# Performance work log

Measured on AMD Instinct MI355X. Metric: run time of the kernel, lower is better.

## Reference

```python
import jax, jax.numpy as jnp
import numpy as np

IN_FEATURES = 4096
OUT_FEATURES = 11008
QMIN, QMAX = -128, 127


def setup_inputs() -> dict:
    key = jax.random.key(0)
    k_in, k_w, k_s, k_z, k_b = jax.random.split(key, 5)
    inp = jax.random.normal(k_in, (4, 2048, IN_FEATURES), dtype=jnp.float32)
    # int8 quantized weight in [qmin, qmax]
    weight_quantized = jax.random.randint(
        k_w, (OUT_FEATURES, IN_FEATURES), QMIN, QMAX + 1, dtype=jnp.int32
    ).astype(jnp.int8)
    # per-output-row scale / zero point (shape [out, 1] as in the module)
    weight_scale = jax.random.uniform(k_s, (OUT_FEATURES, 1), dtype=jnp.float32,
                                      minval=0.005, maxval=0.02)
    weight_zero_point = jax.random.uniform(k_z, (OUT_FEATURES, 1), dtype=jnp.float32,
                                           minval=-4.0, maxval=4.0)
    bias = jax.random.normal(k_b, (OUT_FEATURES,), dtype=jnp.float32) * 0.01
    return {
        "input": inp,
        "weight_quantized": weight_quantized,
        "weight_scale": weight_scale,
        "weight_zero_point": weight_zero_point,
        "bias": bias,
    }


def reference(input, weight_quantized, weight_scale, weight_zero_point, bias):
    # Dequantize: per-row affine, W_f32[o, i] = (q[o, i] - zp[o]) * scale[o]
    weight_float = (weight_quantized.astype(jnp.float32) - weight_zero_point) * weight_scale
    # F.linear: y = x @ W^T + b   -> [B, S, out]
    out = jnp.einsum("bsi,oi->bso", input, weight_float) + bias
    return out
```

## Files before the change

kernel.cpp:

```cpp
#include <hip/hip_runtime.h>

#define K_DIM 4096
#define N_DIM 11008
#define M_DIM 8192
#define NT 64

typedef _Float16 f16;
typedef f16 f16x4 __attribute__((ext_vector_type(4)));
typedef f16 f16x8 __attribute__((ext_vector_type(8)));
typedef float f32x4 __attribute__((ext_vector_type(4)));

typedef __attribute__((address_space(1))) unsigned int gu32;
typedef __attribute__((address_space(3))) unsigned int lu32;

__device__ __forceinline__ void g2l16(const void* gp, void* lp) {
    __builtin_amdgcn_global_load_lds((gu32*)gp, (lu32*)lp, 16, 0, 0);
}

__global__ __launch_bounds__(256) void convw_kernel(const int* __restrict__ Wq,
                                                    f16* __restrict__ Wh) {
    const size_t n4 = (size_t)N_DIM * K_DIM / 4;
    const size_t stride = (size_t)gridDim.x * 256;
    const int4* src = (const int4*)Wq;
    f16x4* dst = (f16x4*)Wh;
    for (size_t i = (size_t)blockIdx.x * 256 + threadIdx.x; i < n4; i += stride) {
        int4 a = src[i];
        f16x4 o = {(f16)a.x, (f16)a.y, (f16)a.z, (f16)a.w};
        dst[i] = o;
    }
}

__global__ __launch_bounds__(256) void convx_kernel(const float* __restrict__ X,
                                                    f16* __restrict__ Xh,
                                                    float* __restrict__ rs) {
    const int row = blockIdx.x;
    const int t = threadIdx.x;
    const float4* xr = (const float4*)(X + (size_t)row * K_DIM);
    f16x4* xo = (f16x4*)(Xh + (size_t)row * K_DIM);
    float s = 0.f;
#pragma unroll
    for (int j = 0; j < 4; ++j) {
        float4 v = xr[t + 256 * j];
        f16x4 h = {(f16)v.x, (f16)v.y, (f16)v.z, (f16)v.w};
        xo[t + 256 * j] = h;
        s += (float)h[0] + (float)h[1] + (float)h[2] + (float)h[3];
    }
#pragma unroll
    for (int off = 32; off > 0; off >>= 1) s += __shfl_down(s, off);
    __shared__ float part[4];
    if ((t & 63) == 0) part[t >> 6] = s;
    __syncthreads();
    if (t == 0) rs[row] = part[0] + part[1] + part[2] + part[3];
}

__global__ __launch_bounds__(512, 2)
void qlin_gemm(const f16* __restrict__ Xh, const f16* __restrict__ Wh,
               const float* __restrict__ scale, const float* __restrict__ zp,
               const float* __restrict__ bias, const float* __restrict__ rowsum,
               float* __restrict__ out) {
    extern __shared__ __align__(16) char smem[];

    const int t = threadIdx.x;
    const int l = t & 63;
    const int w = t >> 6;
    const int wm = w >> 2;
    const int wn = w & 3;
    const int q = l >> 4;
    const int ln = l & 15;

    const int m0 = blockIdx.x * 256;
    const int n0 = blockIdx.y * 256;

    const int srow = t >> 3;
    const int sslot = (t & 7) ^ (srow & 7);
    const char* xbase = (const char*)Xh + ((size_t)(m0 + srow) << 13) + (sslot << 4);
    const char* wbase = (const char*)Wh + ((size_t)(n0 + srow) << 13) + (sslot << 4);
    char* ldst = smem + t * 16;

#define STG_A(p, c, T) g2l16(xbase + ((size_t)(c) << 19) + ((size_t)(T) << 7), ldst + (p)*65536 + (c)*8192)
#define STG_B(p, c, T) g2l16(wbase + ((size_t)(c) << 19) + ((size_t)(T) << 7), ldst + (p)*65536 + 32768 + (c)*8192)
#define SB __builtin_amdgcn_sched_barrier(0)
#define BAR __builtin_amdgcn_s_barrier()
#define LGKM0 asm volatile("s_waitcnt lgkmcnt(0)" ::: "memory")
#define VMC6 asm volatile("s_waitcnt vmcnt(6)" ::: "memory")

    const int xs = ln & 7;
    int offA[2], offB[2];
    offA[0] = (wm * 128 + ln) * 128 + ((q ^ xs) << 4);
    offA[1] = (wm * 128 + ln) * 128 + (((q + 4) ^ xs) << 4);
    offB[0] = 32768 + (wn * 64 + ln) * 128 + ((q ^ xs) << 4);
    offB[1] = 32768 + (wn * 64 + ln) * 128 + (((q + 4) ^ xs) << 4);

    f32x4 acc[8][4] = {};
    f16x8 aR[4][2], b01[2][2], b23[2][2];

#define RD_ALO(P)                                                              \
    _Pragma("unroll") for (int kk = 0; kk < 2; ++kk)                           \
    _Pragma("unroll") for (int i = 0; i < 4; ++i)                              \
        aR[i][kk] = *(const f16x8*)(smem + (P)*65536 + offA[kk] + i * 2048)
#define RD_AHI(P)                                                              \
    _Pragma("unroll") for (int kk = 0; kk < 2; ++kk)                           \
    _Pragma("unroll") for (int i = 0; i < 4; ++i)                              \
        aR[i][kk] = *(const f16x8*)(smem + (P)*65536 + offA[kk] + (4 + i) * 2048)
#define RD_B01(P)                                                              \
    _Pragma("unroll") for (int kk = 0; kk < 2; ++kk)                           \
    _Pragma("unroll") for (int j = 0; j < 2; ++j)                              \
        b01[j][kk] = *(const f16x8*)(smem + (P)*65536 + offB[kk] + j * 2048)
#define RD_B23(P)                                                              \
    _Pragma("unroll") for (int kk = 0; kk < 2; ++kk)                           \
    _Pragma("unroll") for (int j = 0; j < 2; ++j)                              \
        b23[j][kk] = *(const f16x8*)(smem + (P)*65536 + offB[kk] + (2 + j) * 2048)
#define MFMA_BLK(I0, J0, BSET)                                                 \
    _Pragma("unroll") for (int kk = 0; kk < 2; ++kk)                           \
    _Pragma("unroll") for (int i = 0; i < 4; ++i)                              \
    _Pragma("unroll") for (int j = 0; j < 2; ++j)                              \
        acc[(I0) + i][(J0) + j] = __builtin_amdgcn_mfma_f32_16x16x32_f16(      \
            aR[i][kk], BSET[j][kk], acc[(I0) + i][(J0) + j], 0, 0, 0)

    STG_A(0, 0, 0); STG_A(0, 2, 0); STG_B(0, 0, 0); STG_B(0, 1, 0);
    STG_A(0, 1, 0); STG_A(0, 3, 0); STG_B(0, 2, 0); STG_B(0, 3, 0);
    STG_A(1, 0, 1); STG_A(1, 2, 1); STG_B(1, 0, 1); STG_B(1, 1, 1);
    STG_A(1, 1, 1); STG_A(1, 3, 1);
    VMC6; SB; BAR; SB;
    RD_ALO(0); RD_B01(0);
    STG_B(1, 2, 1); STG_B(1, 3, 1);
    LGKM0; SB; BAR; SB;

#define BODY(T, CUR)                                                           \
                          \
    RD_B23(CUR);                                                               \
    MFMA_BLK(0, 0, b01);                                                       \
    STG_A(CUR, 0, (T) + 2); STG_A(CUR, 2, (T) + 2);                            \
    LGKM0; SB; BAR; SB;                                                        \
              \
    MFMA_BLK(0, 2, b23);                                                       \
    RD_AHI(CUR);                                                               \
    STG_B(CUR, 0, (T) + 2); STG_B(CUR, 1, (T) + 2);                            \
    LGKM0; SB; BAR; SB;                                                        \
                 \
    MFMA_BLK(4, 2, b23);                                                       \
    STG_A(CUR, 1, (T) + 2); STG_A(CUR, 3, (T) + 2);                            \
    VMC6; SB; BAR; SB;                                                         \
         \
    MFMA_BLK(4, 0, b01);                                                       \
    RD_ALO((CUR) ^ 1); RD_B01((CUR) ^ 1);                                      \
    STG_B(CUR, 2, (T) + 2); STG_B(CUR, 3, (T) + 2);                            \
    LGKM0; SB; BAR; SB;

#pragma unroll 1
    for (int Tp = 0; Tp < 31; ++Tp) {
        const int Tb = 2 * Tp;
        BODY(Tb, 0);
        BODY(Tb + 1, 1);
    }
#undef BODY

    RD_B23(0);
    MFMA_BLK(0, 0, b01);
    MFMA_BLK(0, 2, b23);
    RD_AHI(0);
    MFMA_BLK(4, 2, b23);
    asm volatile("s_waitcnt vmcnt(0)" ::: "memory");
    SB; BAR; SB;
    MFMA_BLK(4, 0, b01);
    RD_ALO(1); RD_B01(1); RD_B23(1);
    MFMA_BLK(0, 0, b01);
    MFMA_BLK(0, 2, b23);
    RD_AHI(1);
    MFMA_BLK(4, 2, b23);
    MFMA_BLK(4, 0, b01);

    float sc[4], zv[4], bv[4];
    int ncol[4];
#pragma unroll
    for (int j = 0; j < 4; ++j) {
        const int n = n0 + wn * 64 + j * 16 + ln;
        ncol[j] = n;
        sc[j] = scale[n];
        zv[j] = zp[n];
        bv[j] = bias[n];
    }
#pragma unroll
    for (int i = 0; i < 8; ++i) {
#pragma unroll
        for (int r = 0; r < 4; ++r) {
            const int m = m0 + wm * 128 + i * 16 + q * 4 + r;
            const float rsm = rowsum[m];
            const size_t rowoff = (size_t)m * N_DIM;
#pragma unroll
            for (int j = 0; j < 4; ++j) {
                out[rowoff + ncol[j]] = sc[j] * (acc[i][j][r] - zv[j] * rsm) + bv[j];
            }
        }
    }
}

extern "C" void kernel_launch(void* const* d_in, const int* in_sizes, int n_in,
                              void* d_out, int out_size, void* d_ws, size_t ws_size,
                              hipStream_t stream) {
    const float* X     = (const float*)d_in[0];
    const int*   Wq    = (const int*)d_in[1];
    const float* scale = (const float*)d_in[2];
    const float* zp    = (const float*)d_in[3];
    const float* bias  = (const float*)d_in[4];
    float* out = (float*)d_out;

    f16* Wh = (f16*)d_ws;
    f16* Xh = (f16*)((char*)d_ws + (size_t)N_DIM * K_DIM * 2);
    float* rowsum = (float*)((char*)d_ws + (size_t)N_DIM * K_DIM * 2 + (size_t)M_DIM * K_DIM * 2);

    static bool attr_done = false;
    if (!attr_done) {
        (void)hipFuncSetAttribute((const void*)qlin_gemm,
                                  hipFuncAttributeMaxDynamicSharedMemorySize, 131072);
        attr_done = true;
    }

    convw_kernel<<<4096, 256, 0, stream>>>(Wq, Wh);
    convx_kernel<<<M_DIM, 256, 0, stream>>>(X, Xh, rowsum);

    dim3 grid(M_DIM / 256, N_DIM / 256);
    qlin_gemm<<<grid, 512, 131072, stream>>>(Xh, Wh, scale, zp, bias, rowsum, out);
}
```

Baseline: 1.103 ms.

## Restructure main loop into two phases with double-buffered B fragment registers

Reworks the main K-loop schedule. Each tile now runs two barrier phases instead of four, and A-low, A-high and double-buffered B fragments are held in separate register sets, so the next tile's LDS reads can be issued while the current tile's MFMAs run. Global-to-LDS staging is regrouped and the vmcnt wait threshold changes. The aim is to cut barrier count and expose more overlap between LDS reads and MFMA. In exchange it uses noticeably more VGPRs, which may cause spills or lower occupancy.

```diff
diff --git a/kernel.cpp b/kernel.cpp
--- a/kernel.cpp
+++ b/kernel.cpp
@@ -82,7 +82,7 @@
 #define SB __builtin_amdgcn_sched_barrier(0)
 #define BAR __builtin_amdgcn_s_barrier()
 #define LGKM0 asm volatile("s_waitcnt lgkmcnt(0)" ::: "memory")
-#define VMC6 asm volatile("s_waitcnt vmcnt(6)" ::: "memory")
+#define VMC4 asm volatile("s_waitcnt vmcnt(4)" ::: "memory")
 
     const int xs = ln & 7;
     int offA[2], offB[2];
@@ -92,83 +92,76 @@
     offB[1] = 32768 + (wn * 64 + ln) * 128 + (((q + 4) ^ xs) << 4);
 
     f32x4 acc[8][4] = {};
-    f16x8 aR[4][2], b01[2][2], b23[2][2];
-
-#define RD_ALO(P)                                                              \
+    f16x8 aL[4][2], aH[4][2];
+    f16x8 b01A[2][2], b23A[2][2], b01B[2][2], b23B[2][2];
+
+#define RD_AL(P)                                                               \
     _Pragma("unroll") for (int kk = 0; kk < 2; ++kk)                           \
     _Pragma("unroll") for (int i = 0; i < 4; ++i)                              \
-        aR[i][kk] = *(const f16x8*)(smem + (P)*65536 + offA[kk] + i * 2048)
-#define RD_AHI(P)                                                              \
+        aL[i][kk] = *(const f16x8*)(smem + (P)*65536 + offA[kk] + i * 2048)
+#define RD_AH(P)                                                               \
     _Pragma("unroll") for (int kk = 0; kk < 2; ++kk)                           \
     _Pragma("unroll") for (int i = 0; i < 4; ++i)                              \
-        aR[i][kk] = *(const f16x8*)(smem + (P)*65536 + offA[kk] + (4 + i) * 2048)
-#define RD_B01(P)                                                              \
+        aH[i][kk] = *(const f16x8*)(smem + (P)*65536 + offA[kk] + (4 + i) * 2048)
+#define RD_B01(P, D)                                                           \
     _Pragma("unroll") for (int kk = 0; kk < 2; ++kk)                           \
     _Pragma("unroll") for (int j = 0; j < 2; ++j)                              \
-        b01[j][kk] = *(const f16x8*)(smem + (P)*65536 + offB[kk] + j * 2048)
-#define RD_B23(P)                                                              \
+        D[j][kk] = *(const f16x8*)(smem + (P)*65536 + offB[kk] + j * 2048)
+#define RD_B23(P, D)                                                           \
     _Pragma("unroll") for (int kk = 0; kk < 2; ++kk)                           \
     _Pragma("unroll") for (int j = 0; j < 2; ++j)                              \
-        b23[j][kk] = *(const f16x8*)(smem + (P)*65536 + offB[kk] + (2 + j) * 2048)
-#define MFMA_BLK(I0, J0, BSET)                                                 \
+        D[j][kk] = *(const f16x8*)(smem + (P)*65536 + offB[kk] + (2 + j) * 2048)
+#define MFMA_BLK(I0, J0, ASET, BSET)                                           \
     _Pragma("unroll") for (int kk = 0; kk < 2; ++kk)                           \
     _Pragma("unroll") for (int i = 0; i < 4; ++i)                              \
     _Pragma("unroll") for (int j = 0; j < 2; ++j)                              \
         acc[(I0) + i][(J0) + j] = __builtin_amdgcn_mfma_f32_16x16x32_f16(      \
-            aR[i][kk], BSET[j][kk], acc[(I0) + i][(J0) + j], 0, 0, 0)
-
-    STG_A(0, 0, 0); STG_A(0, 2, 0); STG_B(0, 0, 0); STG_B(0, 1, 0);
-    STG_A(0, 1, 0); STG_A(0, 3, 0); STG_B(0, 2, 0); STG_B(0, 3, 0);
-    STG_A(1, 0, 1); STG_A(1, 2, 1); STG_B(1, 0, 1); STG_B(1, 1, 1);
-    STG_A(1, 1, 1); STG_A(1, 3, 1);
-    VMC6; SB; BAR; SB;
-    RD_ALO(0); RD_B01(0);
-    STG_B(1, 2, 1); STG_B(1, 3, 1);
+            ASET[i][kk], BSET[j][kk], acc[(I0) + i][(J0) + j], 0, 0, 0)
+
+    STG_B(0, 0, 0); STG_B(0, 1, 0); STG_B(0, 2, 0); STG_B(0, 3, 0);
+    STG_A(0, 0, 0); STG_A(0, 1, 0); STG_A(0, 2, 0); STG_A(0, 3, 0);
+    STG_B(1, 0, 1); STG_B(1, 1, 1); STG_B(1, 2, 1); STG_B(1, 3, 1);
+    VMC4; SB; BAR; SB;
+    RD_AL(0); RD_B01(0, b01A); RD_B23(0, b23A);
+    STG_A(1, 0, 1); STG_A(1, 1, 1); STG_A(1, 2, 1); STG_A(1, 3, 1);
     LGKM0; SB; BAR; SB;
 
-#define BODY(T, CUR)                                                           \
-                          \
-    RD_B23(CUR);                                                               \
-    MFMA_BLK(0, 0, b01);                                                       \
-    STG_A(CUR, 0, (T) + 2); STG_A(CUR, 2, (T) + 2);                            \
-    LGKM0; SB; BAR; SB;                                                        \
-              \
-    MFMA_BLK(0, 2, b23);                                                       \
-    RD_AHI(CUR);                                                               \
+#define BODY(T, CUR, BS, BD)                                                   \
+                            \
+    RD_AH(CUR);                                                                \
+    MFMA_BLK(0, 0, aL, b01##BS);                                               \
+    MFMA_BLK(0, 2, aL, b23##BS);                                               \
     STG_B(CUR, 0, (T) + 2); STG_B(CUR, 1, (T) + 2);                            \
-    LGKM0; SB; BAR; SB;                                                        \
-                 \
-    MFMA_BLK(4, 2, b23);                                                       \
-    STG_A(CUR, 1, (T) + 2); STG_A(CUR, 3, (T) + 2);                            \
-    VMC6; SB; BAR; SB;                                                         \
-         \
-    MFMA_BLK(4, 0, b01);                                                       \
-    RD_ALO((CUR) ^ 1); RD_B01((CUR) ^ 1);                                      \
     STG_B(CUR, 2, (T) + 2); STG_B(CUR, 3, (T) + 2);                            \
+    VMC4; LGKM0; SB; BAR; SB;                                                  \
+       \
+    RD_AL((CUR) ^ 1); RD_B01((CUR) ^ 1, b01##BD); RD_B23((CUR) ^ 1, b23##BD);  \
+    MFMA_BLK(4, 2, aH, b23##BS);                                               \
+    MFMA_BLK(4, 0, aH, b01##BS);                                               \
+    STG_A(CUR, 0, (T) + 2); STG_A(CUR, 1, (T) + 2);                            \
+    STG_A(CUR, 2, (T) + 2); STG_A(CUR, 3, (T) + 2);                            \
     LGKM0; SB; BAR; SB;
 
 #pragma unroll 1
     for (int Tp = 0; Tp < 31; ++Tp) {
-        const int Tb = 2 * Tp;
-        BODY(Tb, 0);
-        BODY(Tb + 1, 1);
+        BODY(2 * Tp, 0, A, B);
+        BODY(2 * Tp + 1, 1, B, A);
     }
 #undef BODY
 
-    RD_B23(0);
-    MFMA_BLK(0, 0, b01);
-    MFMA_BLK(0, 2, b23);
-    RD_AHI(0);
-    MFMA_BLK(4, 2, b23);
+    RD_AH(0);
+    MFMA_BLK(0, 0, aL, b01A);
+    MFMA_BLK(0, 2, aL, b23A);
     asm volatile("s_waitcnt vmcnt(0)" ::: "memory");
-    SB; BAR; SB;
-    MFMA_BLK(4, 0, b01);
-    RD_ALO(1); RD_B01(1); RD_B23(1);
-    MFMA_BLK(0, 0, b01);
-    MFMA_BLK(0, 2, b23);
-    RD_AHI(1);
-    MFMA_BLK(4, 2, b23);
-    MFMA_BLK(4, 0, b01);
+    LGKM0; SB; BAR; SB;
+    RD_AL(1); RD_B01(1, b01B); RD_B23(1, b23B);
+    MFMA_BLK(4, 2, aH, b23A);
+    MFMA_BLK(4, 0, aH, b01A);
+    RD_AH(1);
+    MFMA_BLK(0, 0, aL, b01B);
+    MFMA_BLK(0, 2, aL, b23B);
+    MFMA_BLK(4, 2, aH, b23B);
+    MFMA_BLK(4, 0, aH, b01B);
 
     float sc[4], zv[4], bv[4];
     int ncol[4];
```

After: 1.105 ms. About the same (+0.2%).
